# Performance work log

Hardware: AMD Instinct MI355X
Metric: run time of the kernel (lower is better)

Reference implementation:

```python
import jax, jax.numpy as jnp
import numpy as np

HIDDEN = 1024
NUM_CLASSES = 10
NUM_GAUSSIANS = 8
IN_FEATURES = 16
HEADS = NUM_CLASSES * NUM_GAUSSIANS * IN_FEATURES * 2  # 2560 tiny Linear(hidden,1) heads


def setup_inputs() -> dict:
    key = jax.random.key(0)
    kx, kw, kb = jax.random.split(key, 3)
    x = jax.random.normal(kx, (8192, HIDDEN), dtype=jnp.float32)
    # Stacked weights of the 2560 per-head Linear(hidden,1) layers.
    bound = 1.0 / np.sqrt(HIDDEN)
    W = jax.random.uniform(kw, (HIDDEN, HEADS), minval=-bound, maxval=bound, dtype=jnp.float32)
    b = jax.random.uniform(kb, (HEADS,), minval=-bound, maxval=bound, dtype=jnp.float32)
    return {"x": x, "W": W, "b": b}


def reference(x, W, b):
    batch = x.shape[0]
    # Fused form of the Python loop of Linear(hidden,1)+Sigmoid per head.
    z = jax.nn.sigmoid(x @ W + b)  # [batch, HEADS]
    return z.reshape(batch, NUM_CLASSES, NUM_GAUSSIANS, IN_FEATURES, 2)
```

## Files before the change

### kernel.cpp

```cpp
#include <hip/hip_runtime.h>
#include <hip/hip_bf16.h>

#define HIDDEN 1024
#define HEADS  2560

#define BM 256
#define BN 320
#define BK 64
#define NT (HIDDEN / BK)
#define ABYTES (BM * BK * 2)
#define BBYTES (BN * BK * 2)
#define BUFSZ  (ABYTES + BBYTES)

typedef float  f32x4  __attribute__((ext_vector_type(4)));
typedef __bf16 bf16x8 __attribute__((ext_vector_type(8)));
typedef __bf16 bf16x4 __attribute__((ext_vector_type(4)));

__device__ __forceinline__ void gload_lds16(const void* g, void* l) {
    __builtin_amdgcn_global_load_lds(
        (const __attribute__((address_space(1))) unsigned int*)g,
        (__attribute__((address_space(3))) unsigned int*)l, 16, 0, 0);
}
__device__ __forceinline__ unsigned swz(unsigned x) {
    return x ^ (((x >> 7) & 7u) << 4);
}

__global__ __launch_bounds__(256)
void cvt_x(const float* __restrict__ x, __bf16* __restrict__ xc, int n8)
{
    int idx = blockIdx.x * blockDim.x + threadIdx.x;
    int stride = gridDim.x * blockDim.x;
    for (int i = idx; i < n8; i += stride) {
        const float4 a = *reinterpret_cast<const float4*>(x + (size_t)i * 8);
        const float4 b = *reinterpret_cast<const float4*>(x + (size_t)i * 8 + 4);
        bf16x8 h;
        h[0] = (__bf16)a.x; h[1] = (__bf16)a.y; h[2] = (__bf16)a.z; h[3] = (__bf16)a.w;
        h[4] = (__bf16)b.x; h[5] = (__bf16)b.y; h[6] = (__bf16)b.z; h[7] = (__bf16)b.w;
        *reinterpret_cast<bf16x8*>(xc + (size_t)i * 8) = h;
    }
}

__global__ __launch_bounds__(256)
void cvt_w(const float* __restrict__ W, __bf16* __restrict__ Wt)
{
    __shared__ __bf16 tile[64][72];
    const int t  = threadIdx.x;
    const int n0 = blockIdx.x * 64;
    const int k0 = blockIdx.y * 64;

    #pragma unroll
    for (int i = 0; i < 4; ++i) {
        const int k    = (t >> 4) + i * 16;
        const int col4 = (t & 15) * 4;
        const float4 v = *reinterpret_cast<const float4*>(
            W + (size_t)(k0 + k) * HEADS + n0 + col4);
        bf16x4 h;
        h[0] = (__bf16)v.x; h[1] = (__bf16)v.y; h[2] = (__bf16)v.z; h[3] = (__bf16)v.w;
        *reinterpret_cast<bf16x4*>(&tile[k][col4]) = h;
    }
    __syncthreads();
    #pragma unroll
    for (int i = 0; i < 4; ++i) {
        const int n  = (t >> 4) + i * 16;
        const int k4 = (t & 15) * 4;
        bf16x4 h;
        h[0] = tile[k4 + 0][n]; h[1] = tile[k4 + 1][n];
        h[2] = tile[k4 + 2][n]; h[3] = tile[k4 + 3][n];
        *reinterpret_cast<bf16x4*>(Wt + (size_t)(n0 + n) * HIDDEN + k0 + k4) = h;
    }
}

__global__ __launch_bounds__(512, 2)
void gemm_dl(const __bf16* __restrict__ A, const __bf16* __restrict__ Bt,
             const float* __restrict__ bias, float* __restrict__ out)
{
    __shared__ char lds[2 * BUFSZ];

    const int t    = threadIdx.x;
    const int lane = t & 63;
    const int w    = t >> 6;
    const int wr   = w >> 2;
    const int wc   = w & 3;
    const int lhi  = lane >> 4;
    const int llo  = lane & 15;

    const int by  = blockIdx.x & 7;
    const int bx  = blockIdx.x >> 3;
    const int bm0 = bx * BM;
    const int bn0 = by * BN;

    const unsigned d0 = (unsigned)(t * 16);
    const unsigned L0 = swz(d0);
    const char* asrc0 = (const char*)A  + (size_t)(bm0 + (L0 >> 7)) * (HIDDEN * 2) + (L0 & 127);
    const char* bsrc0 = (const char*)Bt + (size_t)(bn0 + (L0 >> 7)) * (HIDDEN * 2) + (L0 & 127);
    char* adst0 = (char*)lds + d0;
    char* bdst0 = (char*)lds + ABYTES + d0;

    const unsigned xa   = (unsigned)((llo & 7) << 4);
    const unsigned klo0 = ((unsigned)(lhi * 16)) ^ xa;
    const unsigned klo1 = ((unsigned)(64 + lhi * 16)) ^ xa;
    unsigned offA[8], offB[5];
    #pragma unroll
    for (int m = 0; m < 8; ++m)
        offA[m] = (unsigned)((wr * 128 + m * 16 + llo) * 128);
    #pragma unroll
    for (int n = 0; n < 5; ++n)
        offB[n] = (unsigned)ABYTES + (unsigned)((wc * 80 + n * 16 + llo) * 128);

    f32x4 acc[8][5];
    #pragma unroll
    for (int m = 0; m < 8; ++m)
        #pragma unroll
        for (int n = 0; n < 5; ++n)
            acc[m][n] = f32x4{0.f, 0.f, 0.f, 0.f};

    #pragma unroll
    for (int li = 0; li < 4; ++li) gload_lds16(asrc0 + li * 131072, adst0 + li * 8192);
    #pragma unroll
    for (int li = 0; li < 5; ++li) gload_lds16(bsrc0 + li * 131072, bdst0 + li * 8192);
    asm volatile("s_waitcnt vmcnt(0)" ::: "memory");
    __builtin_amdgcn_s_barrier();

    for (int k = 0; k < NT; ++k) {
        const char* buf  = lds + (k & 1) * BUFSZ;
        const unsigned nb = (unsigned)(((k + 1) & 1) * BUFSZ);
        const int   koff = (k + 1) * 128;

        if (k + 1 < NT) {
            #pragma unroll
            for (int li = 0; li < 4; ++li)
                gload_lds16(asrc0 + li * 131072 + koff, adst0 + nb + li * 8192);
            #pragma unroll
            for (int li = 0; li < 5; ++li)
                gload_lds16(bsrc0 + li * 131072 + koff, bdst0 + nb + li * 8192);
        }

        {
            bf16x8 af[8], bfr[5];
            #pragma unroll
            for (int m = 0; m < 8; ++m) af[m]  = *(const bf16x8*)(buf + (offA[m] + klo0));
            #pragma unroll
            for (int n = 0; n < 5; ++n) bfr[n] = *(const bf16x8*)(buf + (offB[n] + klo0));
            #pragma unroll
            for (int m = 0; m < 8; ++m)
                #pragma unroll
                for (int n = 0; n < 5; ++n)
                    acc[m][n] = __builtin_amdgcn_mfma_f32_16x16x32_bf16(
                        af[m], bfr[n], acc[m][n], 0, 0, 0);
        }
        {
            bf16x8 af[8], bfr[5];
            #pragma unroll
            for (int m = 0; m < 8; ++m) af[m]  = *(const bf16x8*)(buf + (offA[m] + klo1));
            #pragma unroll
            for (int n = 0; n < 5; ++n) bfr[n] = *(const bf16x8*)(buf + (offB[n] + klo1));
            #pragma unroll
            for (int m = 0; m < 8; ++m)
                #pragma unroll
                for (int n = 0; n < 5; ++n)
                    acc[m][n] = __builtin_amdgcn_mfma_f32_16x16x32_bf16(
                        af[m], bfr[n], acc[m][n], 0, 0, 0);
        }

        asm volatile("s_waitcnt vmcnt(0)" ::: "memory");
        __builtin_amdgcn_s_barrier();
    }

    #pragma unroll
    for (int n = 0; n < 5; ++n) {
        const int col  = bn0 + wc * 80 + n * 16 + llo;
        const float bv = bias[col];
        #pragma unroll
        for (int m = 0; m < 8; ++m) {
            const int row0 = bm0 + wr * 128 + m * 16 + lhi * 4;
            #pragma unroll
            for (int r = 0; r < 4; ++r) {
                const float z = acc[m][n][r] + bv;
                out[(size_t)(row0 + r) * HEADS + col] = __fdividef(1.0f, 1.0f + __expf(-z));
            }
        }
    }
}

#define FBM 128
#define FBN 128
#define FBK 32
#define FLDK 40

__global__ __launch_bounds__(256)
void lch_gemm(const float* __restrict__ x, const float* __restrict__ W,
              const float* __restrict__ b, float* __restrict__ out)
{
    __shared__ __bf16 As[FBM][FLDK];
    __shared__ __bf16 Bs[FBN][FLDK];

    const int t   = threadIdx.x;
    const int bm0 = blockIdx.x * FBM;
    const int bn0 = blockIdx.y * FBN;
    const int lane = t & 63;
    const int wid  = t >> 6;
    const int wr   = wid >> 1;
    const int wc   = wid & 1;
    const int lhi  = lane >> 4;
    const int llo  = lane & 15;

    f32x4 acc[4][4];
    #pragma unroll
    for (int i = 0; i < 4; ++i)
        #pragma unroll
        for (int j = 0; j < 4; ++j)
            acc[i][j] = f32x4{0.f, 0.f, 0.f, 0.f};

    const int bn_col  = t & 127;
    const int bk_base = (t >> 7) * 16;

    for (int k0 = 0; k0 < HIDDEN; k0 += FBK) {
        #pragma unroll
        for (int i = 0; i < 4; ++i) {
            const int f   = t + i * 256;
            const int row = f >> 3;
            const int c4  = (f & 7) * 4;
            const float4 v = *reinterpret_cast<const float4*>(
                x + (size_t)(bm0 + row) * HIDDEN + k0 + c4);
            bf16x4 h;
            h[0] = (__bf16)v.x; h[1] = (__bf16)v.y;
            h[2] = (__bf16)v.z; h[3] = (__bf16)v.w;
            *reinterpret_cast<bf16x4*>(&As[row][c4]) = h;
        }
        {
            const float* wp = W + (size_t)(k0 + bk_base) * HEADS + bn0 + bn_col;
            bf16x8 h0, h1;
            #pragma unroll
            for (int i = 0; i < 8; ++i) h0[i] = (__bf16)wp[(size_t)i * HEADS];
            #pragma unroll
            for (int i = 0; i < 8; ++i) h1[i] = (__bf16)wp[(size_t)(i + 8) * HEADS];
            *reinterpret_cast<bf16x8*>(&Bs[bn_col][bk_base])     = h0;
            *reinterpret_cast<bf16x8*>(&Bs[bn_col][bk_base + 8]) = h1;
        }
        __syncthreads();

        bf16x8 af[4], bfr[4];
        #pragma unroll
        for (int i = 0; i < 4; ++i)
            af[i] = *reinterpret_cast<const bf16x8*>(&As[wr * 64 + i * 16 + llo][lhi * 8]);
        #pragma unroll
        for (int j = 0; j < 4; ++j)
            bfr[j] = *reinterpret_cast<const bf16x8*>(&Bs[wc * 64 + j * 16 + llo][lhi * 8]);
        #pragma unroll
        for (int i = 0; i < 4; ++i)
            #pragma unroll
            for (int j = 0; j < 4; ++j)
                acc[i][j] = __builtin_amdgcn_mfma_f32_16x16x32_bf16(
                    af[i], bfr[j], acc[i][j], 0, 0, 0);
        __syncthreads();
    }

    #pragma unroll
    for (int j = 0; j < 4; ++j) {
        const int col  = bn0 + wc * 64 + j * 16 + llo;
        const float bv = b[col];
        #pragma unroll
        for (int i = 0; i < 4; ++i) {
            const int row0 = bm0 + wr * 64 + i * 16 + lhi * 4;
            #pragma unroll
            for (int r = 0; r < 4; ++r) {
                const float z = acc[i][j][r] + bv;
                out[(size_t)(row0 + r) * HEADS + col] = 1.0f / (1.0f + __expf(-z));
            }
        }
    }
}

extern "C" void kernel_launch(void* const* d_in, const int* in_sizes, int n_in,
                              void* d_out, int out_size, void* d_ws, size_t ws_size,
                              hipStream_t stream) {
    const float* x = (const float*)d_in[0];
    const float* W = (const float*)d_in[1];
    const float* b = (const float*)d_in[2];
    float* out     = (float*)d_out;

    const int M = in_sizes[0] / HIDDEN;

    const size_t xc_bytes = (size_t)M * HIDDEN * sizeof(__bf16);
    const size_t wt_bytes = (size_t)HEADS * HIDDEN * sizeof(__bf16);

    if (ws_size >= xc_bytes + wt_bytes && (M % BM) == 0) {
        __bf16* xc = (__bf16*)d_ws;
        __bf16* Wt = (__bf16*)((char*)d_ws + xc_bytes);

        cvt_x<<<2048, 256, 0, stream>>>(x, xc, M * HIDDEN / 8);
        cvt_w<<<dim3(HEADS / 64, HIDDEN / 64), 256, 0, stream>>>(W, Wt);

        const int nwg = (M / BM) * (HEADS / BN);
        gemm_dl<<<nwg, 512, 0, stream>>>(xc, Wt, b, out);
    } else {
        dim3 grid(M / FBM, HEADS / FBN);
        lch_gemm<<<grid, dim3(256), 0, stream>>>(x, W, b, out);
    }
}
```

Baseline: 67.01 us.

## Shrink GEMM tiles to 128x160, fuse conversion kernels, remap block order

Merges the x and W bf16 conversion kernels into one launch, which removes a kernel launch and lets both conversions overlap. Shrinks the GEMM tile from 256x320 to 128x160 with 8 waves each holding 2x5 MFMA accumulators, and raises the occupancy hint to 4 blocks per CU. The grid grows from 256 to 1024 workgroups, so the 256 CUs are spread more evenly. The price is more redundant global and LDS traffic per FLOP and lower register reuse per wave.

```diff
diff --git a/kernel.cpp b/kernel.cpp
--- a/kernel.cpp
+++ b/kernel.cpp
@@ -4,13 +4,13 @@
 #define HIDDEN 1024
 #define HEADS  2560
 
-#define BM 256
-#define BN 320
+#define BM 128
+#define BN 160
 #define BK 64
 #define NT (HIDDEN / BK)
-#define ABYTES (BM * BK * 2)
-#define BBYTES (BN * BK * 2)
-#define BUFSZ  (ABYTES + BBYTES)
+#define ABYT (BM * BK * 2)
+#define BBYT (BN * BK * 2)
+#define BUFSZ (ABYT + BBYT)
 
 typedef float  f32x4  __attribute__((ext_vector_type(4)));
 typedef __bf16 bf16x8 __attribute__((ext_vector_type(8)));
@@ -26,66 +26,66 @@
 }
 
 __global__ __launch_bounds__(256)
-void cvt_x(const float* __restrict__ x, __bf16* __restrict__ xc, int n8)
+void cvt_all(const float* __restrict__ x, const float* __restrict__ W,
+             __bf16* __restrict__ xc, __bf16* __restrict__ Wt, int n8)
 {
-    int idx = blockIdx.x * blockDim.x + threadIdx.x;
-    int stride = gridDim.x * blockDim.x;
-    for (int i = idx; i < n8; i += stride) {
-        const float4 a = *reinterpret_cast<const float4*>(x + (size_t)i * 8);
-        const float4 b = *reinterpret_cast<const float4*>(x + (size_t)i * 8 + 4);
-        bf16x8 h;
-        h[0] = (__bf16)a.x; h[1] = (__bf16)a.y; h[2] = (__bf16)a.z; h[3] = (__bf16)a.w;
-        h[4] = (__bf16)b.x; h[5] = (__bf16)b.y; h[6] = (__bf16)b.z; h[7] = (__bf16)b.w;
-        *reinterpret_cast<bf16x8*>(xc + (size_t)i * 8) = h;
-    }
-}
-
-__global__ __launch_bounds__(256)
-void cvt_w(const float* __restrict__ W, __bf16* __restrict__ Wt)
-{
-    __shared__ __bf16 tile[64][72];
-    const int t  = threadIdx.x;
-    const int n0 = blockIdx.x * 64;
-    const int k0 = blockIdx.y * 64;
-
-    #pragma unroll
-    for (int i = 0; i < 4; ++i) {
-        const int k    = (t >> 4) + i * 16;
-        const int col4 = (t & 15) * 4;
-        const float4 v = *reinterpret_cast<const float4*>(
-            W + (size_t)(k0 + k) * HEADS + n0 + col4);
-        bf16x4 h;
-        h[0] = (__bf16)v.x; h[1] = (__bf16)v.y; h[2] = (__bf16)v.z; h[3] = (__bf16)v.w;
-        *reinterpret_cast<bf16x4*>(&tile[k][col4]) = h;
-    }
-    __syncthreads();
-    #pragma unroll
-    for (int i = 0; i < 4; ++i) {
-        const int n  = (t >> 4) + i * 16;
-        const int k4 = (t & 15) * 4;
-        bf16x4 h;
-        h[0] = tile[k4 + 0][n]; h[1] = tile[k4 + 1][n];
-        h[2] = tile[k4 + 2][n]; h[3] = tile[k4 + 3][n];
-        *reinterpret_cast<bf16x4*>(Wt + (size_t)(n0 + n) * HIDDEN + k0 + k4) = h;
-    }
-}
-
-__global__ __launch_bounds__(512, 2)
-void gemm_dl(const __bf16* __restrict__ A, const __bf16* __restrict__ Bt,
-             const float* __restrict__ bias, float* __restrict__ out)
+    if (blockIdx.x < 640) {
+        __shared__ __bf16 tile[64][72];
+        const int t  = threadIdx.x;
+        const int n0 = (blockIdx.x % 40) * 64;
+        const int k0 = (blockIdx.x / 40) * 64;
+
+        #pragma unroll
+        for (int i = 0; i < 4; ++i) {
+            const int k    = (t >> 4) + i * 16;
+            const int col4 = (t & 15) * 4;
+            const float4 v = *reinterpret_cast<const float4*>(
+                W + (size_t)(k0 + k) * HEADS + n0 + col4);
+            bf16x4 h;
+            h[0] = (__bf16)v.x; h[1] = (__bf16)v.y; h[2] = (__bf16)v.z; h[3] = (__bf16)v.w;
+            *reinterpret_cast<bf16x4*>(&tile[k][col4]) = h;
+        }
+        __syncthreads();
+        #pragma unroll
+        for (int i = 0; i < 4; ++i) {
+            const int n  = (t >> 4) + i * 16;
+            const int k4 = (t & 15) * 4;
+            bf16x4 h;
+            h[0] = tile[k4 + 0][n]; h[1] = tile[k4 + 1][n];
+            h[2] = tile[k4 + 2][n]; h[3] = tile[k4 + 3][n];
+            *reinterpret_cast<bf16x4*>(Wt + (size_t)(n0 + n) * HIDDEN + k0 + k4) = h;
+        }
+    } else {
+        int idx    = (blockIdx.x - 640) * blockDim.x + threadIdx.x;
+        int stride = (gridDim.x - 640) * blockDim.x;
+        for (int i = idx; i < n8; i += stride) {
+            const float4 a = *reinterpret_cast<const float4*>(x + (size_t)i * 8);
+            const float4 b = *reinterpret_cast<const float4*>(x + (size_t)i * 8 + 4);
+            bf16x8 h;
+            h[0] = (__bf16)a.x; h[1] = (__bf16)a.y; h[2] = (__bf16)a.z; h[3] = (__bf16)a.w;
+            h[4] = (__bf16)b.x; h[5] = (__bf16)b.y; h[6] = (__bf16)b.z; h[7] = (__bf16)b.w;
+            *reinterpret_cast<bf16x8*>(xc + (size_t)i * 8) = h;
+        }
+    }
+}
+
+__global__ __launch_bounds__(512, 4)
+void gemm_dl2(const __bf16* __restrict__ A, const __bf16* __restrict__ Bt,
+              const float* __restrict__ bias, float* __restrict__ out)
 {
     __shared__ char lds[2 * BUFSZ];
 
     const int t    = threadIdx.x;
     const int lane = t & 63;
     const int w    = t >> 6;
-    const int wr   = w >> 2;
-    const int wc   = w & 3;
+    const int wr   = w & 3;
+    const int wc   = w >> 2;
     const int lhi  = lane >> 4;
     const int llo  = lane & 15;
 
-    const int by  = blockIdx.x & 7;
-    const int bx  = blockIdx.x >> 3;
+    const int bid = blockIdx.x;
+    const int by  = (bid & 7) * 2 + ((bid >> 3) & 1);
+    const int bx  = bid >> 4;
     const int bm0 = bx * BM;
     const int bn0 = by * BN;
 
@@ -93,31 +93,32 @@
     const unsigned L0 = swz(d0);
     const char* asrc0 = (const char*)A  + (size_t)(bm0 + (L0 >> 7)) * (HIDDEN * 2) + (L0 & 127);
     const char* bsrc0 = (const char*)Bt + (size_t)(bn0 + (L0 >> 7)) * (HIDDEN * 2) + (L0 & 127);
+    const unsigned dt = 16384u + (unsigned)(t * 16);
+    const unsigned Lt = swz(dt);
+    const char* bsrct = (const char*)Bt + (size_t)(bn0 + (Lt >> 7)) * (HIDDEN * 2) + (Lt & 127);
+
     char* adst0 = (char*)lds + d0;
-    char* bdst0 = (char*)lds + ABYTES + d0;
-
-    const unsigned xa   = (unsigned)((llo & 7) << 4);
-    const unsigned klo0 = ((unsigned)(lhi * 16)) ^ xa;
-    const unsigned klo1 = ((unsigned)(64 + lhi * 16)) ^ xa;
-    unsigned offA[8], offB[5];
-    #pragma unroll
-    for (int m = 0; m < 8; ++m)
-        offA[m] = (unsigned)((wr * 128 + m * 16 + llo) * 128);
-    #pragma unroll
-    for (int n = 0; n < 5; ++n)
-        offB[n] = (unsigned)ABYTES + (unsigned)((wc * 80 + n * 16 + llo) * 128);
-
-    f32x4 acc[8][5];
-    #pragma unroll
-    for (int m = 0; m < 8; ++m)
+    char* bdst0 = (char*)lds + ABYT + d0;
+    char* bdstt = (char*)lds + ABYT + dt;
+
+    const unsigned xa = (unsigned)((llo & 7) << 4);
+    const unsigned klo[2] = { ((unsigned)(lhi * 16)) ^ xa,
+                              ((unsigned)(64 + lhi * 16)) ^ xa };
+    const unsigned rowA = (unsigned)((wr * 32 + llo) * 128);
+    const unsigned rowB = (unsigned)ABYT + (unsigned)((wc * 80 + llo) * 128);
+
+    f32x4 acc[2][5];
+    #pragma unroll
+    for (int m = 0; m < 2; ++m)
         #pragma unroll
         for (int n = 0; n < 5; ++n)
             acc[m][n] = f32x4{0.f, 0.f, 0.f, 0.f};
 
-    #pragma unroll
-    for (int li = 0; li < 4; ++li) gload_lds16(asrc0 + li * 131072, adst0 + li * 8192);
-    #pragma unroll
-    for (int li = 0; li < 5; ++li) gload_lds16(bsrc0 + li * 131072, bdst0 + li * 8192);
+    gload_lds16(asrc0,          adst0);
+    gload_lds16(asrc0 + 131072, adst0 + 8192);
+    gload_lds16(bsrc0,          bdst0);
+    gload_lds16(bsrc0 + 131072, bdst0 + 8192);
+    if (w < 4) gload_lds16(bsrct, bdstt);
     asm volatile("s_waitcnt vmcnt(0)" ::: "memory");
     __builtin_amdgcn_s_barrier();
 
@@ -127,40 +128,29 @@
         const int   koff = (k + 1) * 128;
 
         if (k + 1 < NT) {
-            #pragma unroll
-            for (int li = 0; li < 4; ++li)
-                gload_lds16(asrc0 + li * 131072 + koff, adst0 + nb + li * 8192);
-            #pragma unroll
-            for (int li = 0; li < 5; ++li)
-                gload_lds16(bsrc0 + li * 131072 + koff, bdst0 + nb + li * 8192);
-        }
-
-        {
-            bf16x8 af[8], bfr[5];
-            #pragma unroll
-            for (int m = 0; m < 8; ++m) af[m]  = *(const bf16x8*)(buf + (offA[m] + klo0));
-            #pragma unroll
-            for (int n = 0; n < 5; ++n) bfr[n] = *(const bf16x8*)(buf + (offB[n] + klo0));
-            #pragma unroll
-            for (int m = 0; m < 8; ++m)
+            gload_lds16(asrc0 + koff,          adst0 + nb);
+            gload_lds16(asrc0 + koff + 131072, adst0 + nb + 8192);
+            gload_lds16(bsrc0 + koff,          bdst0 + nb);
+            gload_lds16(bsrc0 + koff + 131072, bdst0 + nb + 8192);
+            if (w < 4) gload_lds16(bsrct + koff, bdstt + nb);
+        }
+
+        #pragma unroll
+        for (int kk = 0; kk < 2; ++kk) {
+            bf16x8 af[2], bfr[5];
+            #pragma unroll
+            for (int m = 0; m < 2; ++m)
+                af[m]  = *(const bf16x8*)(buf + rowA + m * 2048 + klo[kk]);
+            #pragma unroll
+            for (int n = 0; n < 5; ++n)
+                bfr[n] = *(const bf16x8*)(buf + rowB + n * 2048 + klo[kk]);
+            #pragma unroll
+            for (int m = 0; m < 2; ++m)
                 #pragma unroll
                 for (int n = 0; n < 5; ++n)
                     acc[m][n] = __builtin_amdgcn_mfma_f32_16x16x32_bf16(
                         af[m], bfr[n], acc[m][n], 0, 0, 0);
         }
-        {
-            bf16x8 af[8], bfr[5];
-            #pragma unroll
-            for (int m = 0; m < 8; ++m) af[m]  = *(const bf16x8*)(buf + (offA[m] + klo1));
-            #pragma unroll
-            for (int n = 0; n < 5; ++n) bfr[n] = *(const bf16x8*)(buf + (offB[n] + klo1));
-            #pragma unroll
-            for (int m = 0; m < 8; ++m)
-                #pragma unroll
-                for (int n = 0; n < 5; ++n)
-                    acc[m][n] = __builtin_amdgcn_mfma_f32_16x16x32_bf16(
-                        af[m], bfr[n], acc[m][n], 0, 0, 0);
-        }
 
         asm volatile("s_waitcnt vmcnt(0)" ::: "memory");
         __builtin_amdgcn_s_barrier();
@@ -171,8 +161,8 @@
         const int col  = bn0 + wc * 80 + n * 16 + llo;
         const float bv = bias[col];
         #pragma unroll
-        for (int m = 0; m < 8; ++m) {
-            const int row0 = bm0 + wr * 128 + m * 16 + lhi * 4;
+        for (int m = 0; m < 2; ++m) {
+            const int row0 = bm0 + wr * 32 + m * 16 + lhi * 4;
             #pragma unroll
             for (int r = 0; r < 4; ++r) {
                 const float z = acc[m][n][r] + bv;
@@ -288,11 +278,10 @@
         __bf16* xc = (__bf16*)d_ws;
         __bf16* Wt = (__bf16*)((char*)d_ws + xc_bytes);
 
-        cvt_x<<<2048, 256, 0, stream>>>(x, xc, M * HIDDEN / 8);
-        cvt_w<<<dim3(HEADS / 64, HIDDEN / 64), 256, 0, stream>>>(W, Wt);
+        cvt_all<<<640 + 2048, 256, 0, stream>>>(x, W, xc, Wt, M * HIDDEN / 8);
 
         const int nwg = (M / BM) * (HEADS / BN);
-        gemm_dl<<<nwg, 512, 0, stream>>>(xc, Wt, b, out);
+        gemm_dl2<<<nwg, 512, 0, stream>>>(xc, Wt, b, out);
     } else {
         dim3 grid(M / FBM, HEADS / FBN);
         lch_gemm<<<grid, dim3(256), 0, stream>>>(x, W, b, out);
```

After: 66.83 us, median of 2. No clear change (-0.3%).
